# Optimization experiments

Hardware: AMD Instinct MI355X
Metric: run time of the kernel (lower is better)

The kernel has to match this reference:

```python
import jax, jax.numpy as jnp
import numpy as np

EPS = 1e-6

def fexp(x, p):
    # signed power used in superquadric parametrization
    return jnp.sign(x) * (jnp.abs(x) + EPS) ** p

def quat_to_rot(q):
    q = q / (jnp.linalg.norm(q, axis=-1, keepdims=True) + EPS)
    w, x, y, z = q[..., 0], q[..., 1], q[..., 2], q[..., 3]
    R = jnp.stack([
        jnp.stack([1 - 2 * (y * y + z * z), 2 * (x * y - w * z), 2 * (x * z + w * y)], -1),
        jnp.stack([2 * (x * y + w * z), 1 - 2 * (x * x + z * z), 2 * (y * z - w * x)], -1),
        jnp.stack([2 * (x * z - w * y), 2 * (y * z + w * x), 1 - 2 * (x * x + y * y)], -1),
    ], -2)
    return R  # (..., 3, 3)

def setup_inputs() -> dict:
    key = jax.random.key(0)
    ks = jax.random.split(key, 9)
    B, M, S, N = 8, 16, 100, 2048
    pcl = jax.random.normal(ks[0], (B, N, 3), jnp.float32)
    translations = 0.5 * jax.random.normal(ks[1], (B, M, 3), jnp.float32)
    rotations = jax.random.normal(ks[2], (B, M, 4), jnp.float32)
    size = 0.2 + 0.6 * jax.random.uniform(ks[3], (B, M, 3), jnp.float32)
    shape_eps = 0.4 + 1.2 * jax.random.uniform(ks[4], (B, M, 2), jnp.float32)
    deformations = 0.6 * jax.random.uniform(ks[5], (B, M, 2), jnp.float32) - 0.3
    probabilities = jax.random.uniform(ks[6], (B, M), jnp.float32, 0.05, 0.95)
    etas = jax.random.uniform(ks[7], (S,), jnp.float32, -np.pi / 2, np.pi / 2)
    omegas = jax.random.uniform(ks[8], (S,), jnp.float32, -np.pi, np.pi)
    return {"pcl": pcl, "translations": translations, "rotations": rotations,
            "size": size, "shape_eps": shape_eps, "deformations": deformations,
            "probabilities": probabilities, "etas": etas, "omegas": omegas}

def reference(pcl, translations, rotations, size, shape_eps, deformations, probabilities, etas, omegas):
    B, N, _ = pcl.shape
    M = translations.shape[1]
    # transform pcl into primitive-centric frames: (B,N,M,3)
    R = quat_to_rot(rotations)                                   # (B,M,3,3)
    d = pcl[:, :, None, :] - translations[:, None, :, :]         # (B,N,M,3)
    pcl_t = jnp.einsum('bmij,bnmj->bnmi', R, d)                  # (B,N,M,3)
    # sample superquadric surfaces: (B,M,S,3)
    e1 = shape_eps[..., 0:1]; e2 = shape_eps[..., 1:2]           # (B,M,1)
    a1 = size[..., 0:1]; a2 = size[..., 1:2]; a3 = size[..., 2:3]
    ce = fexp(jnp.cos(etas)[None, None, :], e1)
    se = fexp(jnp.sin(etas)[None, None, :], e1)
    cw = fexp(jnp.cos(omegas)[None, None, :], e2)
    sw = fexp(jnp.sin(omegas)[None, None, :], e2)
    x = a1 * ce * cw; y = a2 * ce * sw; z = a3 * se              # (B,M,S)
    # tapering deformation
    fx = deformations[..., 0:1] * z / a3 + 1.0
    fy = deformations[..., 1:2] * z / a3 + 1.0
    points = jnp.stack([fx * x, fy * y, z], -1)                  # (B,M,S,3)
    # pairwise squared distances: (B,M,S,N)
    diff = points[:, :, :, None, :] - jnp.transpose(pcl_t, (0, 2, 1, 3))[:, :, None, :, :]
    dist = jnp.sum(diff * diff, -1)
    # --- pcl_to_prim loss ---
    dmin = jnp.transpose(jnp.min(dist, axis=2), (0, 2, 1))       # (B,N,M)
    idx = jnp.argsort(dmin, axis=-1)
    distance = jnp.take_along_axis(dmin, idx, axis=-1)
    probs_g = jax.vmap(lambda p, i: p[i])(probabilities, idx)    # (B,N,M)
    neg_cp = jnp.cumprod(1.0 - probs_g, axis=-1)
    neg_cp = jnp.concatenate([jnp.ones_like(neg_cp[..., :1]), neg_cp[..., :-1]], -1)
    minprob = probs_g * neg_cp
    pcl_to_prim = jnp.sum(distance * minprob) / (B * N)
    # --- prim_to_pcl loss ---
    dminN = jnp.min(dist, axis=3)                                # (B,M,S)
    dminN = jnp.where(dminN >= 1e30, 0.0, dminN)
    s0, s1, s2 = size[..., 0], size[..., 1], size[..., 2]
    area = 4 * np.pi * ((s0 * s1) ** 1.6 / 3 + (s0 * s2) ** 1.6 / 3 + (s1 * s2) ** 1.6 / 3) ** 0.625
    area = M * area / jnp.sum(area, axis=-1, keepdims=True)
    prim_to_pcl = jnp.sum(jnp.mean(dminN, -1) * area) / (B * M)
    # regularizer weights are zero (regularizer_type=None path) -> regs = 0
    return pcl_to_prim + prim_to_pcl
```

## Files before the change

### kernel.cpp

```cpp
#include <hip/hip_runtime.h>
#include <math.h>

#define EPSF 1e-6f

constexpr int B = 8, N = 2048, M = 16, S = 100;
constexpr int MAIN_BLOCKS = B * (N / 64);
constexpr int PRIM_BLOCKS = B * M * 2;
constexpr int TOTAL_BLOCKS = MAIN_BLOCKS + PRIM_BLOCKS;

__device__ __forceinline__ float fexp_d(float x, float p) {
    float sg = (x > 0.f) ? 1.f : ((x < 0.f) ? -1.f : 0.f);
    return sg * __powf(fabsf(x) + EPSF, p);
}

__device__ __forceinline__ void quat_R(const float* __restrict__ rot, int bm, float R[9]) {
    float w = rot[bm * 4 + 0], x = rot[bm * 4 + 1], y = rot[bm * 4 + 2], z = rot[bm * 4 + 3];
    float inv = 1.0f / (sqrtf(w * w + x * x + y * y + z * z) + EPSF);
    w *= inv; x *= inv; y *= inv; z *= inv;
    R[0] = 1.f - 2.f * (y * y + z * z); R[1] = 2.f * (x * y - w * z); R[2] = 2.f * (x * z + w * y);
    R[3] = 2.f * (x * y + w * z); R[4] = 1.f - 2.f * (x * x + z * z); R[5] = 2.f * (y * z - w * x);
    R[6] = 2.f * (x * z - w * y); R[7] = 2.f * (y * z + w * x); R[8] = 1.f - 2.f * (x * x + y * y);
}

__device__ __forceinline__ float4 surf_point(
    const float* __restrict__ sizep, const float* __restrict__ seps,
    const float* __restrict__ deform, const float* __restrict__ etas,
    const float* __restrict__ omegas, int bm, int s)
{
    float e1 = seps[bm * 2 + 0], e2 = seps[bm * 2 + 1];
    float a1 = sizep[bm * 3 + 0], a2 = sizep[bm * 3 + 1], a3 = sizep[bm * 3 + 2];
    float d0 = deform[bm * 2 + 0], d1 = deform[bm * 2 + 1];
    float se_, ce_, sw_, cw_;
    __sincosf(etas[s], &se_, &ce_);
    __sincosf(omegas[s], &sw_, &cw_);
    float ce = fexp_d(ce_, e1);
    float se = fexp_d(se_, e1);
    float cw = fexp_d(cw_, e2);
    float sw = fexp_d(sw_, e2);
    float x = a1 * ce * cw;
    float y = a2 * ce * sw;
    float z = a3 * se;
    float fx = d0 * (z / a3) + 1.0f;
    float fy = d1 * (z / a3) + 1.0f;
    float4 P;
    P.x = fx * x; P.y = fy * y; P.z = z;
    P.w = P.x * P.x + P.y * P.y + P.z * P.z;
    return P;
}

__global__ __launch_bounds__(256) void k_all(
    const float* __restrict__ pcl, const float* __restrict__ trans,
    const float* __restrict__ rot, const float* __restrict__ sizep,
    const float* __restrict__ seps, const float* __restrict__ deform,
    const float* __restrict__ probs,
    const float* __restrict__ etas, const float* __restrict__ omegas,
    float* __restrict__ out)
{
    __shared__ float4 pts[S * M];
    __shared__ float sbuf[20];

    int t = threadIdx.x;

    if (blockIdx.x < MAIN_BLOCKS) {
        int b  = blockIdx.x >> 5;
        int n0 = (blockIdx.x & 31) * 64;

        for (int i = t; i < S * M; i += 256) {
            int s = i >> 4, m = i & 15;
            pts[i] = surf_point(sizep, seps, deform, etas, omegas, b * M + m, s);
        }
        __syncthreads();

        int m  = t & 15;
        int nl = t >> 4;
        int bm = b * M + m;
        float R[9];
        quat_R(rot, bm, R);
        float tx = trans[bm * 3 + 0], ty = trans[bm * 3 + 1], tz = trans[bm * 3 + 2];

        float mx[4], my[4], mz[4], psq[4], dmin[4];
#pragma unroll
        for (int j = 0; j < 4; j++) {
            int n = n0 + nl + 16 * j;
            float px = pcl[(b * N + n) * 3 + 0];
            float py = pcl[(b * N + n) * 3 + 1];
            float pz = pcl[(b * N + n) * 3 + 2];
            float dx = px - tx, dy = py - ty, dz = pz - tz;
            float X = R[0] * dx + R[1] * dy + R[2] * dz;
            float Y = R[3] * dx + R[4] * dy + R[5] * dz;
            float Z = R[6] * dx + R[7] * dy + R[8] * dz;
            mx[j] = -2.f * X; my[j] = -2.f * Y; mz[j] = -2.f * Z;
            psq[j] = X * X + Y * Y + Z * Z;
            dmin[j] = 3.4e38f;
        }

        for (int s = 0; s < S; s++) {
            float4 P = pts[s * M + m];
#pragma unroll
            for (int j = 0; j < 4; j++) {
                float d = fmaf(P.x, mx[j], P.w);
                d = fmaf(P.y, my[j], d);
                d = fmaf(P.z, mz[j], d);
                dmin[j] = fminf(dmin[j], d);
            }
        }

        float pv  = probs[bm];
        float acc = 0.f;
#pragma unroll
        for (int j = 0; j < 4; j++) {
            float key = dmin[j] + psq[j];
            float prod = 1.f;
#pragma unroll
            for (int k = 0; k < 16; k++) {
                float bk = __shfl(key, k, 16);
                bool before = (bk < key) || (bk == key && k < m);
                float omp = 1.f - probs[b * M + k];
                prod *= before ? omp : 1.f;
            }
            acc += key * pv * prod;
        }
        for (int off = 32; off >= 1; off >>= 1) acc += __shfl_down(acc, off);
        if ((t & 63) == 0) atomicAdd(out, acc * (1.0f / (B * N)));
    } else {
        int pb = blockIdx.x - MAIN_BLOCKS;
        int bm = pb >> 1, q = pb & 1;
        int b = bm >> 4, m = bm & 15;
        int s0 = q * 50;

        float4* spts = pts;
        float* sarea = sbuf;
        float* wsum  = sbuf + 16;

        if (t < 50) spts[t] = surf_point(sizep, seps, deform, etas, omegas, bm, s0 + t);
        if (t >= 64 && t < 64 + M) {
            int mm = t - 64;
            float s0s = sizep[(b * M + mm) * 3 + 0];
            float s1s = sizep[(b * M + mm) * 3 + 1];
            float s2s = sizep[(b * M + mm) * 3 + 2];
            float tt = __powf(s0s * s1s, 1.6f) / 3.f + __powf(s0s * s2s, 1.6f) / 3.f
                     + __powf(s1s * s2s, 1.6f) / 3.f;
            sarea[mm] = 4.0f * 3.14159265358979323846f * __powf(tt, 0.625f);
        }
        __syncthreads();

        float R[9];
        quat_R(rot, bm, R);
        float tx = trans[bm * 3 + 0], ty = trans[bm * 3 + 1], tz = trans[bm * 3 + 2];

        int w = t >> 6, lane = t & 63;
        int cnt = (w < 2) ? 13 : 12;
        int off = (w < 2) ? w * 13 : 26 + (w - 2) * 12;

        float px[13], py[13], pz[13], mins[13];
#pragma unroll
        for (int k = 0; k < 13; k++) {
            int sl = (k < cnt) ? (off + k) : off;
            float4 P = spts[sl];
            px[k] = P.x; py[k] = P.y; pz[k] = P.z;
            mins[k] = 3.4e38f;
        }

        for (int i = 0; i < 32; i++) {
            int n = i * 64 + lane;
            const float* pp = pcl + (b * N + n) * 3;
            float dx = pp[0] - tx, dy = pp[1] - ty, dz = pp[2] - tz;
            float X = R[0] * dx + R[1] * dy + R[2] * dz;
            float Y = R[3] * dx + R[4] * dy + R[5] * dz;
            float Z = R[6] * dx + R[7] * dy + R[8] * dz;
            float mX = -2.f * X, mY = -2.f * Y, mZ = -2.f * Z;
            float Xsq = X * X + Y * Y + Z * Z;
#pragma unroll
            for (int k = 0; k < 13; k++) {
                float d = fmaf(px[k], mX, Xsq);
                d = fmaf(py[k], mY, d);
                d = fmaf(pz[k], mZ, d);
                mins[k] = fminf(mins[k], d);
            }
        }

        float sum = 0.f;
#pragma unroll
        for (int k = 0; k < 13; k++) {
            float v = mins[k];
            for (int o = 32; o >= 1; o >>= 1) v = fminf(v, __shfl_down(v, o));
            int sl = (k < cnt) ? (off + k) : off;
            v += spts[sl].w;
            sum += (k < cnt) ? v : 0.f;
        }

        if (lane == 0) wsum[w] = sum;
        __syncthreads();
        if (t == 0) {
            float total = wsum[0] + wsum[1] + wsum[2] + wsum[3];
            float asum = 0.f;
            for (int mm = 0; mm < M; mm++) asum += sarea[mm];
            float area = (float)M * sarea[m] / asum;
            atomicAdd(out, total * area * (1.0f / (S * B * M)));
        }
    }
}

extern "C" void kernel_launch(void* const* d_in, const int* in_sizes, int n_in,
                              void* d_out, int out_size, void* d_ws, size_t ws_size,
                              hipStream_t stream)
{
    const float* pcl    = (const float*)d_in[0];
    const float* trans  = (const float*)d_in[1];
    const float* rot    = (const float*)d_in[2];
    const float* sizep  = (const float*)d_in[3];
    const float* seps   = (const float*)d_in[4];
    const float* deform = (const float*)d_in[5];
    const float* probs  = (const float*)d_in[6];
    const float* etas   = (const float*)d_in[7];
    const float* omegas = (const float*)d_in[8];
    float* out = (float*)d_out;

    k_all<<<TOTAL_BLOCKS, 256, 0, stream>>>(pcl, trans, rot, sizep, seps, deform,
                                            probs, etas, omegas, out);
}
```

Measured before the change: 104.0 us.

## Replace global atomics with partial buffer plus reduce kernel; prefetch loads

```diff
diff --git a/kernel.cpp b/kernel.cpp
--- a/kernel.cpp
+++ b/kernel.cpp
@@ -7,6 +7,7 @@
 constexpr int MAIN_BLOCKS = B * (N / 64);
 constexpr int PRIM_BLOCKS = B * M * 2;
 constexpr int TOTAL_BLOCKS = MAIN_BLOCKS + PRIM_BLOCKS;
+constexpr int NPART = MAIN_BLOCKS * 4 + PRIM_BLOCKS;
 
 __device__ __forceinline__ float fexp_d(float x, float p) {
     float sg = (x > 0.f) ? 1.f : ((x < 0.f) ? -1.f : 0.f);
@@ -54,7 +55,7 @@
     const float* __restrict__ seps, const float* __restrict__ deform,
     const float* __restrict__ probs,
     const float* __restrict__ etas, const float* __restrict__ omegas,
-    float* __restrict__ out)
+    float* __restrict__ part)
 {
     __shared__ float4 pts[S * M];
     __shared__ float sbuf[20];
@@ -94,17 +95,33 @@
             dmin[j] = 3.4e38f;
         }
 
-        for (int s = 0; s < S; s++) {
-            float4 P = pts[s * M + m];
-#pragma unroll
-            for (int j = 0; j < 4; j++) {
-                float d = fmaf(P.x, mx[j], P.w);
-                d = fmaf(P.y, my[j], d);
-                d = fmaf(P.z, mz[j], d);
-                dmin[j] = fminf(dmin[j], d);
-            }
-        }
-
+        float4 Pa[4], Pb[4];
+#pragma unroll
+        for (int u = 0; u < 4; u++) Pa[u] = pts[u * M + m];
+        for (int s = 0; s < S; s += 4) {
+#pragma unroll
+            for (int u = 0; u < 4; u++) {
+                int sn = s + 4 + u; if (sn >= S) sn = S - 1;
+                Pb[u] = pts[sn * M + m];
+            }
+#pragma unroll
+            for (int u = 0; u < 4; u++) {
+                float4 P = Pa[u];
+#pragma unroll
+                for (int j = 0; j < 4; j++) {
+                    float d = fmaf(P.x, mx[j], P.w);
+                    d = fmaf(P.y, my[j], d);
+                    d = fmaf(P.z, mz[j], d);
+                    dmin[j] = fminf(dmin[j], d);
+                }
+            }
+#pragma unroll
+            for (int u = 0; u < 4; u++) Pa[u] = Pb[u];
+        }
+
+        float ompr[16];
+#pragma unroll
+        for (int k = 0; k < 16; k++) ompr[k] = 1.f - probs[b * M + k];
         float pv  = probs[bm];
         float acc = 0.f;
 #pragma unroll
@@ -115,13 +132,13 @@
             for (int k = 0; k < 16; k++) {
                 float bk = __shfl(key, k, 16);
                 bool before = (bk < key) || (bk == key && k < m);
-                float omp = 1.f - probs[b * M + k];
-                prod *= before ? omp : 1.f;
+                prod *= before ? ompr[k] : 1.f;
             }
             acc += key * pv * prod;
         }
         for (int off = 32; off >= 1; off >>= 1) acc += __shfl_down(acc, off);
-        if ((t & 63) == 0) atomicAdd(out, acc * (1.0f / (B * N)));
+        if ((t & 63) == 0)
+            part[blockIdx.x * 4 + (t >> 6)] = acc * (1.0f / (B * N));
     } else {
         int pb = blockIdx.x - MAIN_BLOCKS;
         int bm = pb >> 1, q = pb & 1;
@@ -161,10 +178,12 @@
             mins[k] = 3.4e38f;
         }
 
+        const float* pcb = pcl + b * N * 3;
+        float cx = pcb[lane * 3 + 0], cy = pcb[lane * 3 + 1], cz = pcb[lane * 3 + 2];
         for (int i = 0; i < 32; i++) {
-            int n = i * 64 + lane;
-            const float* pp = pcl + (b * N + n) * 3;
-            float dx = pp[0] - tx, dy = pp[1] - ty, dz = pp[2] - tz;
+            int n2 = (i < 31) ? ((i + 1) * 64 + lane) : lane;
+            float nx = pcb[n2 * 3 + 0], ny = pcb[n2 * 3 + 1], nz = pcb[n2 * 3 + 2];
+            float dx = cx - tx, dy = cy - ty, dz = cz - tz;
             float X = R[0] * dx + R[1] * dy + R[2] * dz;
             float Y = R[3] * dx + R[4] * dy + R[5] * dz;
             float Z = R[6] * dx + R[7] * dy + R[8] * dz;
@@ -177,6 +196,7 @@
                 d = fmaf(pz[k], mZ, d);
                 mins[k] = fminf(mins[k], d);
             }
+            cx = nx; cy = ny; cz = nz;
         }
 
         float sum = 0.f;
@@ -196,9 +216,22 @@
             float asum = 0.f;
             for (int mm = 0; mm < M; mm++) asum += sarea[mm];
             float area = (float)M * sarea[m] / asum;
-            atomicAdd(out, total * area * (1.0f / (S * B * M)));
+            part[MAIN_BLOCKS * 4 + pb] = total * area * (1.0f / (S * B * M));
         }
     }
+}
+
+__global__ __launch_bounds__(256) void k_reduce(const float* __restrict__ part,
+                                               float* __restrict__ out)
+{
+    __shared__ float ws[4];
+    int t = threadIdx.x;
+    float s = 0.f;
+    for (int i = t; i < NPART; i += 256) s += part[i];
+    for (int off = 32; off >= 1; off >>= 1) s += __shfl_down(s, off);
+    if ((t & 63) == 0) ws[t >> 6] = s;
+    __syncthreads();
+    if (t == 0) out[0] = ws[0] + ws[1] + ws[2] + ws[3];
 }
 
 extern "C" void kernel_launch(void* const* d_in, const int* in_sizes, int n_in,
@@ -214,8 +247,10 @@
     const float* probs  = (const float*)d_in[6];
     const float* etas   = (const float*)d_in[7];
     const float* omegas = (const float*)d_in[8];
-    float* out = (float*)d_out;
+    float* out  = (float*)d_out;
+    float* partials = (float*)d_ws;
 
     k_all<<<TOTAL_BLOCKS, 256, 0, stream>>>(pcl, trans, rot, sizep, seps, deform,
-                                            probs, etas, omegas, out);
-}
+                                            probs, etas, omegas, partials);
+    k_reduce<<<1, 256, 0, stream>>>(partials, out);
+}
```

Result: faster. 93.10 us (-10.4%).
